# Kernel optimization log

Measured on AMD Instinct MI355X. Metric: run time of the kernel, lower is better.

## Reference

```python
import jax, jax.numpy as jnp
import numpy as np

BLOCK = 16
H = 16
KV = 4
HPG = H // KV
DH = 64
SCALE = 1.0 / np.sqrt(DH).astype(np.float32)


def setup_inputs() -> dict:
    key = jax.random.key(0)
    ks = jax.random.split(key, 7)
    B, Ldec, Lenc, D = 2, 8192, 4096, 1024
    s = 1.0 / np.sqrt(D).astype(np.float32)
    return {
        "hidden_states": jax.random.normal(ks[0], (B, Ldec, D), jnp.float32),
        "encoder_hidden_states": jax.random.normal(ks[1], (B, Lenc, D), jnp.float32),
        "attention_mask": jax.random.randint(ks[2], (B, Lenc), 0, 2, jnp.int32),
        "Wq": jax.random.normal(ks[3], (D, H * DH), jnp.float32) * s,
        "Wk": jax.random.normal(ks[4], (D, KV * DH), jnp.float32) * s,
        "Wv": jax.random.normal(ks[5], (D, KV * DH), jnp.float32) * s,
        "Wo": jax.random.normal(ks[6], (H * DH, D), jnp.float32) * s,
    }


def reference(hidden_states, encoder_hidden_states, attention_mask, Wq, Wk, Wv, Wo):
    B, Ldec, D = hidden_states.shape
    Lenc = encoder_hidden_states.shape[1]
    pad = (BLOCK - Ldec % BLOCK) % BLOCK
    x = jnp.pad(hidden_states, ((0, 0), (0, pad), (0, 0))) if pad else hidden_states
    nb = (Ldec + pad) // BLOCK
    # mean-pool decoder tokens into blocks: [B, nb, D]
    pooled = x.reshape(B, nb, BLOCK, D).mean(axis=2)
    # projections; GQA: group q heads by kv head (repeat_interleave order)
    q = (pooled @ Wq).reshape(B, nb, KV, HPG, DH)          # [B, nb, KV, HPG, DH]
    k = (encoder_hidden_states @ Wk).reshape(B, Lenc, KV, DH)
    v = (encoder_hidden_states @ Wv).reshape(B, Lenc, KV, DH)
    scores = jnp.einsum("bngqd,blgd->bgqnl", q, k) * SCALE  # [B, KV, HPG, nb, Lenc]
    mask = (attention_mask == 0)[:, None, None, None, :]
    scores = jnp.where(mask, jnp.float32(-1e9), scores)
    attn = jax.nn.softmax(scores, axis=-1)
    out = jnp.einsum("bgqnl,blgd->bngqd", attn, v)          # [B, nb, KV, HPG, DH]
    out = out.reshape(B, nb, H * DH) @ Wo                   # [B, nb, D]
    # broadcast block output back to token level
    unpooled = jnp.broadcast_to(out[:, :, None, :], (B, nb, BLOCK, D)).reshape(B, nb * BLOCK, D)
    return unpooled[:, :Ldec, :]
```

## Files before the change

### kernel.cpp

```cpp
#include <hip/hip_runtime.h>


typedef unsigned short u16;
typedef __attribute__((ext_vector_type(8))) __bf16 bf16x8;
typedef __attribute__((ext_vector_type(4))) float f32x4;
typedef __attribute__((ext_vector_type(4))) _Float16 f16x4;

static __device__ __forceinline__ u16 f2bf(float f) {
    unsigned int u = __float_as_uint(f);
    u = (u + 0x7fffu + ((u >> 16) & 1u)) >> 16;
    return (u16)u;
}
static __device__ __forceinline__ void gload16(const u16* g, u16* l) {
    __builtin_amdgcn_global_load_lds(
        (const __attribute__((address_space(1))) void*)g,
        (__attribute__((address_space(3))) void*)l, 16, 0, 0);
}

__global__ __launch_bounds__(256) void prep_all(const float* __restrict__ enc,
                                                const float* __restrict__ hid,
                                                const int* __restrict__ mask,
                                                const float* __restrict__ Wq,
                                                const float* __restrict__ Wk,
                                                const float* __restrict__ Wv,
                                                const float* __restrict__ Wo,
                                                u16* __restrict__ encb,
                                                u16* __restrict__ poolb,
                                                u16* __restrict__ mh,
                                                u16* __restrict__ Wq_t,
                                                u16* __restrict__ Wkv_t,
                                                u16* __restrict__ Wo_t) {
    int bid = blockIdx.x;
    if (bid < 1024) {
        const int row = bid;
        const int c4 = threadIdx.x;
        const float4* src = (const float4*)(hid + (size_t)row * 16 * 1024) + c4;
        float4 v[16];
#pragma unroll
        for (int t = 0; t < 16; ++t) v[t] = src[(size_t)t * 256];
#pragma unroll
        for (int t = 0; t < 8; ++t) {
            v[t].x += v[t + 8].x; v[t].y += v[t + 8].y;
            v[t].z += v[t + 8].z; v[t].w += v[t + 8].w;
        }
#pragma unroll
        for (int t = 0; t < 4; ++t) {
            v[t].x += v[t + 4].x; v[t].y += v[t + 4].y;
            v[t].z += v[t + 4].z; v[t].w += v[t + 4].w;
        }
#pragma unroll
        for (int t = 0; t < 2; ++t) {
            v[t].x += v[t + 2].x; v[t].y += v[t + 2].y;
            v[t].z += v[t + 2].z; v[t].w += v[t + 2].w;
        }
        v[0].x += v[1].x; v[0].y += v[1].y; v[0].z += v[1].z; v[0].w += v[1].w;
        ushort4 o;
        o.x = f2bf(v[0].x * 0.0625f); o.y = f2bf(v[0].y * 0.0625f);
        o.z = f2bf(v[0].z * 0.0625f); o.w = f2bf(v[0].w * 0.0625f);
        *(ushort4*)(poolb + (size_t)row * 1024 + c4 * 4) = o;
    } else if (bid < 2048) {
        const int base = (bid - 1024) * 2048 + threadIdx.x;
        float4 v[8];
#pragma unroll
        for (int j = 0; j < 8; ++j) v[j] = ((const float4*)enc)[base + j * 256];
#pragma unroll
        for (int j = 0; j < 8; ++j) {
            ushort4 o;
            o.x = f2bf(v[j].x); o.y = f2bf(v[j].y);
            o.z = f2bf(v[j].z); o.w = f2bf(v[j].w);
            ((ushort4*)encb)[base + j * 256] = o;
        }
    } else if (bid < 4608) {
        bid -= 2048;
        const float* in; u16* out; int N, nbx, rowoff;
        if (bid < 1024)      { in = Wq; out = Wq_t;  N = 1024; nbx = 32; rowoff = 0; }
        else if (bid < 2048) { in = Wo; out = Wo_t;  N = 1024; nbx = 32; rowoff = 0; bid -= 1024; }
        else if (bid < 2304) { in = Wk; out = Wkv_t; N = 256;  nbx = 8;  rowoff = 0; bid -= 2048; }
        else                 { in = Wv; out = Wkv_t; N = 256;  nbx = 8;  rowoff = 256; bid -= 2304; }
        const int n0 = (bid % nbx) * 32, k0 = (bid / nbx) * 32;
        __shared__ float t[32][33];
        const int tx = threadIdx.x & 31, ty = threadIdx.x >> 5;
#pragma unroll
        for (int i = 0; i < 4; ++i)
            t[ty + 8 * i][tx] = in[(size_t)(k0 + ty + 8 * i) * N + n0 + tx];
        __syncthreads();
#pragma unroll
        for (int i = 0; i < 4; ++i)
            out[(size_t)(rowoff + n0 + ty + 8 * i) * 1024 + k0 + tx] = f2bf(t[tx][ty + 8 * i]);
    } else {
#pragma unroll
        for (int k = 0; k < 32; ++k) {
            const int i = threadIdx.x + 256 * k;
            mh[i] = mask[i] ? (u16)0x3C00 : (u16)0;
        }
    }
}

template <int MODE>
static __device__ __forceinline__ void gemm_core(const u16* __restrict__ A,
                                                 const u16* __restrict__ Bt,
                                                 u16* __restrict__ outQ,
                                                 float* __restrict__ out_f,
                                                 int m0, int n0, int kt0, int nkt,
                                                 u16* sAB) {
    u16* sA = sAB;
    u16* sB = sAB + 64 * 64;
    const int t = threadIdx.x;
    const int w = t >> 6, lane = t & 63, quad = lane >> 4, r16 = lane & 15;
    const int row8 = lane >> 3, seg = lane & 7;

    f32x4 acc[4];
#pragma unroll
    for (int i = 0; i < 4; ++i) acc[i] = (f32x4){0.f, 0.f, 0.f, 0.f};

    for (int kt = kt0; kt < kt0 + nkt; ++kt) {
        const int k0 = kt * 64;
        __syncthreads();
#pragma unroll
        for (int j = 0; j < 2; ++j) {
            const int ra = w * 16 + j * 8;
            gload16(A + (size_t)(m0 + ra + row8) * 1024 + k0 + seg * 8, sA + ra * 64);
            gload16(Bt + (size_t)(n0 + ra + row8) * 1024 + k0 + seg * 8, sB + ra * 64);
        }
        __syncthreads();
#pragma unroll
        for (int kk = 0; kk < 2; ++kk) {
            const bf16x8 af = *(const bf16x8*)(sA + (16 * w + r16) * 64 + kk * 32 + quad * 8);
#pragma unroll
            for (int nt = 0; nt < 4; ++nt) {
                const bf16x8 bfv = *(const bf16x8*)(sB + (nt * 16 + r16) * 64 + kk * 32 + quad * 8);
                acc[nt] = __builtin_amdgcn_mfma_f32_16x16x32_bf16(af, bfv, acc[nt], 0, 0, 0);
            }
        }
    }

    if (MODE == 0) {
#pragma unroll
        for (int nt = 0; nt < 4; ++nt)
#pragma unroll
            for (int r = 0; r < 4; ++r) {
                const int m = m0 + 16 * w + quad * 4 + r;
                const int c = n0 + nt * 16 + r16;
                const int b = m >> 9, nq = m & 511, g = c >> 8, qh = (c >> 6) & 3, d = c & 63;
                outQ[((((size_t)(b * 4 + g) * 4 + qh) * 512 + nq) << 6) + d] =
                    f2bf(acc[nt][r] * 0.180336880f);
            }
    } else {
#pragma unroll
        for (int nt = 0; nt < 4; ++nt)
#pragma unroll
            for (int r = 0; r < 4; ++r) {
                const int m = m0 + 16 * w + quad * 4 + r;
                const int c = n0 + nt * 16 + r16;
                out_f[(size_t)m * 1024 + c] = acc[nt][r];
            }
    }
}

__global__ __launch_bounds__(256) void gemm_qkv(const u16* __restrict__ poolb,
                                                const u16* __restrict__ encb,
                                                const u16* __restrict__ Wq_t,
                                                const u16* __restrict__ Wkv_t,
                                                const int* __restrict__ maskp,
                                                u16* __restrict__ Qa,
                                                u16* __restrict__ Ka,
                                                u16* __restrict__ Va) {
    __shared__ __align__(16) u16 smem[12288];
    const int bx = blockIdx.x;
    if (bx >= 512) {
        const int b = bx - 512;
        gemm_core<0>(poolb, Wq_t, Qa, nullptr, (b >> 4) * 64, (b & 15) * 64, 0, 16, smem);
        return;
    }
    const int m0 = (bx >> 3) * 128, n0 = (bx & 7) * 64;
    u16* sA = smem;
    u16* sB = smem + 128 * 64;
    const int t = threadIdx.x;
    const int w = t >> 6, lane = t & 63, quad = lane >> 4, r16 = lane & 15;
    const int row8 = lane >> 3, seg = lane & 7;

    f32x4 acc[2][4];
#pragma unroll
    for (int i = 0; i < 2; ++i)
#pragma unroll
        for (int nt = 0; nt < 4; ++nt) acc[i][nt] = (f32x4){0.f, 0.f, 0.f, 0.f};

    for (int kt = 0; kt < 16; ++kt) {
        const int k0 = kt * 64;
        __syncthreads();
#pragma unroll
        for (int p = 0; p < 4; ++p) {
            const int ra = p * 32 + w * 8;
            gload16(encb + (size_t)(m0 + ra + row8) * 1024 + k0 + seg * 8, sA + ra * 64);
        }
#pragma unroll
        for (int p = 0; p < 2; ++p) {
            const int ra = p * 32 + w * 8;
            gload16(Wkv_t + (size_t)(n0 + ra + row8) * 1024 + k0 + seg * 8, sB + ra * 64);
        }
        __syncthreads();
#pragma unroll
        for (int kk = 0; kk < 2; ++kk)
#pragma unroll
            for (int i = 0; i < 2; ++i) {
                const bf16x8 af = *(const bf16x8*)(sA + (w * 32 + i * 16 + r16) * 64 + kk * 32 + quad * 8);
#pragma unroll
                for (int nt = 0; nt < 4; ++nt) {
                    const bf16x8 bfv = *(const bf16x8*)(sB + (nt * 16 + r16) * 64 + kk * 32 + quad * 8);
                    acc[i][nt] = __builtin_amdgcn_mfma_f32_16x16x32_bf16(af, bfv, acc[i][nt], 0, 0, 0);
                }
            }
    }

    const bool isV = (n0 >= 256);
    const int g = (isV ? (n0 - 256) : n0) >> 6;
    const int b = m0 >> 12, l0 = m0 & 4095;
    __syncthreads();
    if (isV) {
        u16* sT = smem;
#pragma unroll
        for (int i = 0; i < 2; ++i) {
            float mfl[4];
#pragma unroll
            for (int r = 0; r < 4; ++r)
                mfl[r] = maskp[b * 4096 + l0 + w * 32 + i * 16 + quad * 4 + r] ? 1.f : 0.f;
#pragma unroll
            for (int nt = 0; nt < 4; ++nt)
#pragma unroll
                for (int r = 0; r < 4; ++r) {
                    const int ml = w * 32 + i * 16 + quad * 4 + r, cl = nt * 16 + r16;
                    union { _Float16 h; u16 u; } cv;
                    cv.h = (_Float16)(acc[i][nt][r] * mfl[r]);
                    sT[cl * 136 + ml] = cv.u;
                }
        }
        __syncthreads();
#pragma unroll
        for (int p = 0; p < 4; ++p) {
            const int idx = t + 256 * p, rr = idx >> 4, ch = idx & 15;
            *(int4*)(Va + ((size_t)(b * 4 + g) * 64 + rr) * 4096 + l0 + ch * 8) =
                *(const int4*)(sT + rr * 136 + ch * 8);
        }
    } else {
        u16* sT = smem;
#pragma unroll
        for (int i = 0; i < 2; ++i)
#pragma unroll
            for (int nt = 0; nt < 4; ++nt)
#pragma unroll
                for (int r = 0; r < 4; ++r) {
                    const int ml = w * 32 + i * 16 + quad * 4 + r, cl = nt * 16 + r16;
                    sT[ml * 72 + cl] = f2bf(acc[i][nt][r]);
                }
        __syncthreads();
#pragma unroll
        for (int p = 0; p < 4; ++p) {
            const int idx = t + 256 * p, rr = idx >> 3, ch = idx & 7;
            *(int4*)(Ka + (((size_t)(b * 4 + g) * 4096 + l0 + rr) << 6) + ch * 8) =
                *(const int4*)(sT + rr * 72 + ch * 8);
        }
    }
}

__global__ __launch_bounds__(256) void gemm_o_bcast(const u16* __restrict__ attn,
                                                    const u16* __restrict__ Wo_t,
                                                    float* __restrict__ out) {
    __shared__ __align__(16) u16 smem[2][8192];
    __shared__ __align__(16) float sf[64 * 68];
    const int bx = blockIdx.x;
    const int m0 = (bx >> 4) * 64, n0 = (bx & 15) * 64;
    const int t = threadIdx.x;
    const int w = t >> 6, lane = t & 63, quad = lane >> 4, r16 = lane & 15;
    const int row8 = lane >> 3, seg = lane & 7;

    f32x4 acc[4];
#pragma unroll
    for (int i = 0; i < 4; ++i) acc[i] = (f32x4){0.f, 0.f, 0.f, 0.f};

    auto stage = [&](int kt, int bi) {
        const int k0 = kt * 64;
        u16* sA = smem[bi];
        u16* sB = smem[bi] + 4096;
#pragma unroll
        for (int j = 0; j < 2; ++j) {
            const int ra = w * 16 + j * 8;
            gload16(attn + (size_t)(m0 + ra + row8) * 1024 + k0 + seg * 8, sA + ra * 64);
            gload16(Wo_t + (size_t)(n0 + ra + row8) * 1024 + k0 + seg * 8, sB + ra * 64);
        }
    };
    stage(0, 0);
    for (int kt = 0; kt < 16; ++kt) {
        const int bi = kt & 1;
        __syncthreads();
        if (kt < 15) stage(kt + 1, bi ^ 1);
        const u16* sA = smem[bi];
        const u16* sB = smem[bi] + 4096;
#pragma unroll
        for (int kk = 0; kk < 2; ++kk) {
            const bf16x8 af = *(const bf16x8*)(sA + (16 * w + r16) * 64 + kk * 32 + quad * 8);
#pragma unroll
            for (int nt = 0; nt < 4; ++nt) {
                const bf16x8 bfv = *(const bf16x8*)(sB + (nt * 16 + r16) * 64 + kk * 32 + quad * 8);
                acc[nt] = __builtin_amdgcn_mfma_f32_16x16x32_bf16(af, bfv, acc[nt], 0, 0, 0);
            }
        }
    }
    __syncthreads();
#pragma unroll
    for (int nt = 0; nt < 4; ++nt)
#pragma unroll
        for (int r = 0; r < 4; ++r)
            sf[(16 * w + quad * 4 + r) * 68 + nt * 16 + r16] = acc[nt][r];
    __syncthreads();
    const int rr = t >> 4, ch = t & 15;
#pragma unroll
    for (int i = 0; i < 4; ++i) {
        const int row = i * 16 + rr;
        const int m = m0 + row, b = m >> 9, n = m & 511;
        const float4 v = *(const float4*)(sf + row * 68 + ch * 4);
        float4* dst = (float4*)(out + ((size_t)b * 8192 + (size_t)n * 16) * 1024 + n0) + ch;
#pragma unroll
        for (int rep = 0; rep < 16; ++rep)
            dst[(size_t)rep * 256] = v;
    }
}

__global__ __launch_bounds__(256, 4) void flash_attn(const u16* __restrict__ Qa,
                                                     const u16* __restrict__ Ka,
                                                     const u16* __restrict__ Vt,
                                                     const u16* __restrict__ mh,
                                                     float* __restrict__ Opart,
                                                     float* __restrict__ mlpart) {
    const int bx = blockIdx.x;
    const int s16 = bx & 31, rr = bx >> 5;
    const int split = rr & 3, gb = rr >> 2;
    const int g = gb & 3, b = gb >> 2;
    __shared__ __align__(16) u16 sK[64 * 72];
    __shared__ __align__(16) u16 sV[64 * 68];
    const int t = threadIdx.x;
    const int qh = t >> 6, lane = t & 63, quad = lane >> 4, r16 = lane & 15;

    bf16x8 aq[2];
    {
        const size_t qbase = ((((size_t)(b * 4 + g) * 4 + qh) * 512) + s16 * 16 + r16) * 64;
#pragma unroll
        for (int kk = 0; kk < 2; ++kk)
            aq[kk] = *(const bf16x8*)(Qa + qbase + kk * 32 + quad * 8);
    }
    const u16* Kg = Ka + (size_t)(b * 4 + g) * 4096 * 64 + (size_t)split * 1024 * 64;
    const u16* Vg = Vt + (size_t)(b * 4 + g) * 64 * 4096 + split * 1024;
    const u16* mb = mh + b * 4096 + split * 1024 + quad * 4;

    f32x4 o[4], lacc;
#pragma unroll
    for (int i = 0; i < 4; ++i) o[i] = (f32x4){0.f, 0.f, 0.f, 0.f};
    lacc = (f32x4){0.f, 0.f, 0.f, 0.f};

    for (int tile = 0; tile < 16; ++tile) {
        const int l0 = tile * 64;
        __syncthreads();
#pragma unroll
        for (int p = 0; p < 2; ++p) {
            const int idx = t + 256 * p, row = idx >> 3, seg = idx & 7;
            *(int4*)(sK + row * 72 + seg * 8) =
                *(const int4*)(Kg + (size_t)(l0 + row) * 64 + seg * 8);
            *(int4*)(sV + row * 68 + seg * 8) =
                *(const int4*)(Vg + (size_t)row * 4096 + l0 + seg * 8);
        }
        __syncthreads();

        f32x4 st[4];
#pragma unroll
        for (int nt = 0; nt < 4; ++nt) st[nt] = (f32x4){0.f, 0.f, 0.f, 0.f};
#pragma unroll
        for (int kk = 0; kk < 2; ++kk)
#pragma unroll
            for (int nt = 0; nt < 4; ++nt) {
                const bf16x8 ka = *(const bf16x8*)(sK + (nt * 16 + r16) * 72 + kk * 32 + quad * 8);
                st[nt] = __builtin_amdgcn_mfma_f32_16x16x32_bf16(ka, aq[kk], st[nt], 0, 0, 0);
            }

#pragma unroll
        for (int nt = 0; nt < 4; ++nt) {
            f16x4 pa;
#pragma unroll
            for (int j = 0; j < 4; ++j)
                pa[j] = (_Float16)__builtin_amdgcn_exp2f(st[nt][j]);
            const f16x4 bvm = *(const f16x4*)(mb + l0 + nt * 16);
            lacc = __builtin_amdgcn_mfma_f32_16x16x16f16(pa, bvm, lacc, 0, 0, 0);
#pragma unroll
            for (int dt = 0; dt < 4; ++dt) {
                const f16x4 bv = *(const f16x4*)(sV + (dt * 16 + r16) * 68 + nt * 16 + quad * 4);
                o[dt] = __builtin_amdgcn_mfma_f32_16x16x16f16(pa, bv, o[dt], 0, 0, 0);
            }
        }
    }

    const size_t pbase = ((size_t)bx * 4 + qh) * 1024;
#pragma unroll
    for (int dt = 0; dt < 4; ++dt)
#pragma unroll
        for (int r = 0; r < 4; ++r)
            Opart[pbase + (size_t)(quad * 4 + r) * 64 + dt * 16 + r16] = o[dt][r];
    if (r16 == 0) {
#pragma unroll
        for (int r = 0; r < 4; ++r)
            mlpart[((size_t)bx * 4 + qh) * 16 + quad * 4 + r] = lacc[r];
    }
}

__global__ __launch_bounds__(256) void flash_combine(const float* __restrict__ Opart,
                                                     const float* __restrict__ mlpart,
                                                     u16* __restrict__ attnout) {
    const int bx = blockIdx.x;
    const int s16 = bx & 31, h = bx >> 5;
    const int qh = h & 3, g = (h >> 2) & 3, b = h >> 4;
    const int t = threadIdx.x;
    const int q = t >> 4, dg = t & 15;
    float4 a = make_float4(0.f, 0.f, 0.f, 0.f);
    float L = 0.f;
#pragma unroll
    for (int s = 0; s < 4; ++s) {
        const size_t part = (((size_t)((b * 4 + g) * 4 + s) * 32 + s16) * 4 + qh);
        const float4 v = *(const float4*)(Opart + part * 1024 + q * 64 + dg * 4);
        a.x += v.x; a.y += v.y; a.z += v.z; a.w += v.w;
        L += mlpart[part * 16 + q];
    }
    const float invL = 1.f / L;
    ushort4 ov;
    ov.x = f2bf(a.x * invL); ov.y = f2bf(a.y * invL);
    ov.z = f2bf(a.z * invL); ov.w = f2bf(a.w * invL);
    *(ushort4*)(attnout + ((size_t)b * 512 + s16 * 16 + q) * 1024 +
                (g * 4 + qh) * 64 + dg * 4) = ov;
}

extern "C" void kernel_launch(void* const* d_in, const int* in_sizes, int n_in,
                              void* d_out, int out_size, void* d_ws, size_t ws_size,
                              hipStream_t stream) {
    const float* hid  = (const float*)d_in[0];
    const float* enc  = (const float*)d_in[1];
    const int*   mask = (const int*)d_in[2];
    const float* Wq   = (const float*)d_in[3];
    const float* Wk   = (const float*)d_in[4];
    const float* Wv   = (const float*)d_in[5];
    const float* Wo   = (const float*)d_in[6];
    float* out = (float*)d_out;

    char* ws = (char*)d_ws;
    size_t off = 0;
    auto alloc = [&](size_t bytes) -> char* {
        char* p = ws + off;
        off += (bytes + 255) & ~(size_t)255;
        return p;
    };
    u16* Wq_t  = (u16*)alloc((size_t)1024 * 1024 * 2);
    u16* Wkv_t = (u16*)alloc((size_t)512 * 1024 * 2);
    u16* Wo_t  = (u16*)alloc((size_t)1024 * 1024 * 2);
    u16* encb  = (u16*)alloc((size_t)8192 * 1024 * 2);
    u16* poolb = (u16*)alloc((size_t)1024 * 1024 * 2);
    u16* Qa    = (u16*)alloc((size_t)1024 * 1024 * 2);
    u16* Ka    = (u16*)alloc((size_t)8 * 4096 * 64 * 2);
    u16* Va    = (u16*)alloc((size_t)8 * 4096 * 64 * 2);
    u16* attn  = (u16*)alloc((size_t)1024 * 1024 * 2);
    u16* mh    = (u16*)alloc((size_t)8192 * 2);
    float* Opart  = (float*)encb;
    float* mlpart = (float*)poolb;

    prep_all<<<4609, 256, 0, stream>>>(enc, hid, mask, Wq, Wk, Wv, Wo,
                                       encb, poolb, mh, Wq_t, Wkv_t, Wo_t);
    gemm_qkv<<<768, 256, 0, stream>>>(poolb, encb, Wq_t, Wkv_t, mask, Qa, Ka, Va);
    flash_attn<<<1024, 256, 0, stream>>>(Qa, Ka, Va, mh, Opart, mlpart);
    flash_combine<<<1024, 256, 0, stream>>>(Opart, mlpart, attn);
    gemm_o_bcast<<<256, 256, 0, stream>>>(attn, Wo_t, out);
}
```

Before: 240.8 us.

## Drop split-K attention, fuse normalization, double-buffer K/V tiles through registers

The attention kernel no longer splits the encoder length four ways. Each block now walks all 64 tiles and normalizes and writes the bf16 output directly, so the separate combine kernel and its fp32 partial buffers go away. K/V tiles are prefetched into registers and stored into a second LDS buffer while the current tile is computed, which halves the barriers per tile. The grid shrinks from 1024 to 256 blocks, so the GPU has less parallelism and latency hiding, and each block runs four times longer.

Measured after the change: 261.4 us. +8.6%, slower.

```diff
diff --git a/kernel.cpp b/kernel.cpp
--- a/kernel.cpp
+++ b/kernel.cpp
@@ -325,18 +325,16 @@
     }
 }
 
-__global__ __launch_bounds__(256, 4) void flash_attn(const u16* __restrict__ Qa,
-                                                     const u16* __restrict__ Ka,
-                                                     const u16* __restrict__ Vt,
-                                                     const u16* __restrict__ mh,
-                                                     float* __restrict__ Opart,
-                                                     float* __restrict__ mlpart) {
+__global__ __launch_bounds__(256) void flash_attn(const u16* __restrict__ Qa,
+                                                  const u16* __restrict__ Ka,
+                                                  const u16* __restrict__ Vt,
+                                                  const u16* __restrict__ mh,
+                                                  u16* __restrict__ attnout) {
     const int bx = blockIdx.x;
-    const int s16 = bx & 31, rr = bx >> 5;
-    const int split = rr & 3, gb = rr >> 2;
+    const int s16 = bx & 31, gb = bx >> 5;
     const int g = gb & 3, b = gb >> 2;
-    __shared__ __align__(16) u16 sK[64 * 72];
-    __shared__ __align__(16) u16 sV[64 * 68];
+    __shared__ __align__(16) u16 sK[2][64 * 72];
+    __shared__ __align__(16) u16 sV[2][64 * 68];
     const int t = threadIdx.x;
     const int qh = t >> 6, lane = t & 63, quad = lane >> 4, r16 = lane & 15;
 
@@ -347,27 +345,41 @@
         for (int kk = 0; kk < 2; ++kk)
             aq[kk] = *(const bf16x8*)(Qa + qbase + kk * 32 + quad * 8);
     }
-    const u16* Kg = Ka + (size_t)(b * 4 + g) * 4096 * 64 + (size_t)split * 1024 * 64;
-    const u16* Vg = Vt + (size_t)(b * 4 + g) * 64 * 4096 + split * 1024;
-    const u16* mb = mh + b * 4096 + split * 1024 + quad * 4;
+    const u16* Kg = Ka + (size_t)(b * 4 + g) * 4096 * 64;
+    const u16* Vg = Vt + (size_t)(b * 4 + g) * 64 * 4096;
+    const u16* mb = mh + b * 4096 + quad * 4;
+
+    const int row0 = t >> 3, seg0 = t & 7;
+    const int row1 = (t + 256) >> 3, seg1 = t & 7;
 
     f32x4 o[4], lacc;
 #pragma unroll
     for (int i = 0; i < 4; ++i) o[i] = (f32x4){0.f, 0.f, 0.f, 0.f};
     lacc = (f32x4){0.f, 0.f, 0.f, 0.f};
 
-    for (int tile = 0; tile < 16; ++tile) {
+    int4 rk0, rk1, rv0, rv1;
+    auto ldtile = [&](int l0) {
+        rk0 = *(const int4*)(Kg + (size_t)(l0 + row0) * 64 + seg0 * 8);
+        rk1 = *(const int4*)(Kg + (size_t)(l0 + row1) * 64 + seg1 * 8);
+        rv0 = *(const int4*)(Vg + (size_t)row0 * 4096 + l0 + seg0 * 8);
+        rv1 = *(const int4*)(Vg + (size_t)row1 * 4096 + l0 + seg1 * 8);
+    };
+    auto sttile = [&](int bi) {
+        *(int4*)(sK[bi] + row0 * 72 + seg0 * 8) = rk0;
+        *(int4*)(sK[bi] + row1 * 72 + seg1 * 8) = rk1;
+        *(int4*)(sV[bi] + row0 * 68 + seg0 * 8) = rv0;
+        *(int4*)(sV[bi] + row1 * 68 + seg1 * 8) = rv1;
+    };
+
+    ldtile(0);
+    sttile(0);
+    __syncthreads();
+
+#pragma unroll 2
+    for (int tile = 0; tile < 64; ++tile) {
+        const int bi = tile & 1;
         const int l0 = tile * 64;
-        __syncthreads();
-#pragma unroll
-        for (int p = 0; p < 2; ++p) {
-            const int idx = t + 256 * p, row = idx >> 3, seg = idx & 7;
-            *(int4*)(sK + row * 72 + seg * 8) =
-                *(const int4*)(Kg + (size_t)(l0 + row) * 64 + seg * 8);
-            *(int4*)(sV + row * 68 + seg * 8) =
-                *(const int4*)(Vg + (size_t)row * 4096 + l0 + seg * 8);
-        }
-        __syncthreads();
+        if (tile < 63) ldtile(l0 + 64);
 
         f32x4 st[4];
 #pragma unroll
@@ -376,7 +388,7 @@
         for (int kk = 0; kk < 2; ++kk)
 #pragma unroll
             for (int nt = 0; nt < 4; ++nt) {
-                const bf16x8 ka = *(const bf16x8*)(sK + (nt * 16 + r16) * 72 + kk * 32 + quad * 8);
+                const bf16x8 ka = *(const bf16x8*)(sK[bi] + (nt * 16 + r16) * 72 + kk * 32 + quad * 8);
                 st[nt] = __builtin_amdgcn_mfma_f32_16x16x32_bf16(ka, aq[kk], st[nt], 0, 0, 0);
             }
 
@@ -390,48 +402,24 @@
             lacc = __builtin_amdgcn_mfma_f32_16x16x16f16(pa, bvm, lacc, 0, 0, 0);
 #pragma unroll
             for (int dt = 0; dt < 4; ++dt) {
-                const f16x4 bv = *(const f16x4*)(sV + (dt * 16 + r16) * 68 + nt * 16 + quad * 4);
+                const f16x4 bv = *(const f16x4*)(sV[bi] + (dt * 16 + r16) * 68 + nt * 16 + quad * 4);
                 o[dt] = __builtin_amdgcn_mfma_f32_16x16x16f16(pa, bv, o[dt], 0, 0, 0);
             }
         }
-    }
-
-    const size_t pbase = ((size_t)bx * 4 + qh) * 1024;
-#pragma unroll
-    for (int dt = 0; dt < 4; ++dt)
-#pragma unroll
-        for (int r = 0; r < 4; ++r)
-            Opart[pbase + (size_t)(quad * 4 + r) * 64 + dt * 16 + r16] = o[dt][r];
-    if (r16 == 0) {
-#pragma unroll
-        for (int r = 0; r < 4; ++r)
-            mlpart[((size_t)bx * 4 + qh) * 16 + quad * 4 + r] = lacc[r];
-    }
-}
-
-__global__ __launch_bounds__(256) void flash_combine(const float* __restrict__ Opart,
-                                                     const float* __restrict__ mlpart,
-                                                     u16* __restrict__ attnout) {
-    const int bx = blockIdx.x;
-    const int s16 = bx & 31, h = bx >> 5;
-    const int qh = h & 3, g = (h >> 2) & 3, b = h >> 4;
-    const int t = threadIdx.x;
-    const int q = t >> 4, dg = t & 15;
-    float4 a = make_float4(0.f, 0.f, 0.f, 0.f);
-    float L = 0.f;
-#pragma unroll
-    for (int s = 0; s < 4; ++s) {
-        const size_t part = (((size_t)((b * 4 + g) * 4 + s) * 32 + s16) * 4 + qh);
-        const float4 v = *(const float4*)(Opart + part * 1024 + q * 64 + dg * 4);
-        a.x += v.x; a.y += v.y; a.z += v.z; a.w += v.w;
-        L += mlpart[part * 16 + q];
-    }
-    const float invL = 1.f / L;
-    ushort4 ov;
-    ov.x = f2bf(a.x * invL); ov.y = f2bf(a.y * invL);
-    ov.z = f2bf(a.z * invL); ov.w = f2bf(a.w * invL);
-    *(ushort4*)(attnout + ((size_t)b * 512 + s16 * 16 + q) * 1024 +
-                (g * 4 + qh) * 64 + dg * 4) = ov;
+
+        if (tile < 63) sttile(bi ^ 1);
+        __syncthreads();
+    }
+
+    const size_t obase = ((size_t)b * 512 + s16 * 16) * 1024 + (g * 4 + qh) * 64;
+#pragma unroll
+    for (int r = 0; r < 4; ++r) {
+        const float invL = 1.f / lacc[r];
+        const size_t rbase = obase + (size_t)(quad * 4 + r) * 1024;
+#pragma unroll
+        for (int dt = 0; dt < 4; ++dt)
+            attnout[rbase + dt * 16 + r16] = f2bf(o[dt][r] * invL);
+    }
 }
 
 extern "C" void kernel_launch(void* const* d_in, const int* in_sizes, int n_in,
@@ -463,13 +451,10 @@
     u16* Va    = (u16*)alloc((size_t)8 * 4096 * 64 * 2);
     u16* attn  = (u16*)alloc((size_t)1024 * 1024 * 2);
     u16* mh    = (u16*)alloc((size_t)8192 * 2);
-    float* Opart  = (float*)encb;
-    float* mlpart = (float*)poolb;
 
     prep_all<<<4609, 256, 0, stream>>>(enc, hid, mask, Wq, Wk, Wv, Wo,
                                        encb, poolb, mh, Wq_t, Wkv_t, Wo_t);
     gemm_qkv<<<768, 256, 0, stream>>>(poolb, encb, Wq_t, Wkv_t, mask, Qa, Ka, Va);
-    flash_attn<<<1024, 256, 0, stream>>>(Qa, Ka, Va, mh, Opart, mlpart);
-    flash_combine<<<1024, 256, 0, stream>>>(Opart, mlpart, attn);
+    flash_attn<<<256, 256, 0, stream>>>(Qa, Ka, Va, mh, attn);
     gemm_o_bcast<<<256, 256, 0, stream>>>(attn, Wo_t, out);
 }
```
